# Kernel tuning notes

Measured on AMD Instinct MI355X. Metric: run time of the kernel, lower is better.

Reference implementation:

```python
import jax, jax.numpy as jnp
import numpy as np

NEG_SLOPE = 0.2   # negative_slope
EPS = 1e-6        # leaky-relu eps
BN_EPS = 1e-5     # torch BatchNorm default eps


def setup_inputs() -> dict:
    key = jax.random.key(0)
    k1, k2, k3 = jax.random.split(key, 3)
    B, C_in, C_out, N = 8, 256, 256, 8192
    x = jax.random.normal(k1, (B, C_in, 3, N), dtype=jnp.float32)
    s = 1.0 / np.sqrt(C_in)  # nn.Linear default init range
    W_feat = jax.random.uniform(k2, (C_out, C_in), minval=-s, maxval=s, dtype=jnp.float32)
    W_dir = jax.random.uniform(k3, (C_out, C_in), minval=-s, maxval=s, dtype=jnp.float32)
    gamma = jnp.ones((C_out,), jnp.float32)
    beta = jnp.zeros((C_out,), jnp.float32)
    return {"x": x, "W_feat": W_feat, "W_dir": W_dir, "gamma": gamma, "beta": beta}


def reference(x, W_feat, W_dir, gamma, beta):
    # VNLinear: kron(W, eye(3)) conv2d == per-vector channel mix
    p = jnp.einsum('oc,bcdn->bodn', W_feat, x)  # [B, O, 3, N]

    # VNBatchNorm: BN (training mode, batch stats) on vector norms, then rescale
    norm = jnp.sqrt(jnp.sum(p * p, axis=2))           # [B, O, N]
    mean = jnp.mean(norm, axis=(0, 2))                # [O]
    var = jnp.var(norm, axis=(0, 2))                  # [O] biased, as torch BN
    norm_bn = ((norm - mean[None, :, None]) * jax.lax.rsqrt(var + BN_EPS)[None, :, None]
               * gamma[None, :, None] + beta[None, :, None])
    p = p / norm[:, :, None, :] * norm_bn[:, :, None, :]

    # VNLeakyReLU with direction computed from the ORIGINAL input x
    d = jnp.einsum('oc,bcdn->bodn', W_dir, x)         # [B, O, 3, N]
    dot = jnp.sum(p * d, axis=2, keepdims=True)       # [B, O, 1, N]
    d_norm_sq = jnp.sum(d * d, axis=2, keepdims=True)
    return jnp.where(dot >= 0, p, p - (1.0 - NEG_SLOPE) * (dot / (d_norm_sq + EPS)) * d)
```

## Files before the change

### kernel.cpp

```cpp
#include <hip/hip_runtime.h>
#include <math.h>

#define BDIM 8
#define CIN  256
#define COUT 256
#define NDIM 8192

#define NEG_COEF  0.8f
#define LRELU_EPS 1e-6f
#define BN_EPS    1e-5f

typedef __attribute__((ext_vector_type(8))) short bf16x8;
typedef __attribute__((ext_vector_type(4))) float f32x4;

#define WS_WFH 0
#define WS_WFL 65536
#define WS_WDH 131072
#define WS_WDL 196608
#define WS_STATS_BYTE 524288
#define NSLOT 8
#define TILE_BYTES 12288
#define WS_XHI_BYTE 557056
#define XIMG_BYTES 100663296ull
#define WS_XLO_BYTE (WS_XHI_BYTE + XIMG_BYTES)
#define WS_NEED (WS_XLO_BYTE + XIMG_BYTES)

__device__ __forceinline__ unsigned short f2bf(float f) {
    unsigned u = __float_as_uint(f);
    return (unsigned short)((u + 0x7FFFu + ((u >> 16) & 1u)) >> 16);
}
__device__ __forceinline__ float bf2f(unsigned short h) {
    return __uint_as_float(((unsigned)h) << 16);
}

__device__ __forceinline__ int swz(int off) {
    return off ^ (((off >> 6) & 7) << 4);
}

__device__ __forceinline__ void gl_lds16(const char* g, char* l) {
    __builtin_amdgcn_global_load_lds(
        (const __attribute__((address_space(1))) unsigned int*)g,
        (__attribute__((address_space(3))) unsigned int*)l, 16, 0, 0);
}

__global__ __launch_bounds__(256) void setup_w_kernel(
    const float* __restrict__ Wf, const float* __restrict__ Wd,
    unsigned short* __restrict__ wsu)
{
    const int o = blockIdx.x;
    const int mat = blockIdx.y;
    const int c = threadIdx.x;
    const float* W = mat ? Wd : Wf;
    float w = W[o * CIN + c];
    unsigned short hi = f2bf(w);
    unsigned short lo = f2bf(w - bf2f(hi));
    int pos = (c & ~31) + 4 * (c & 7) + ((c >> 3) & 3);
    unsigned short* ph = wsu + (mat ? WS_WDH : WS_WFH);
    unsigned short* pl = wsu + (mat ? WS_WDL : WS_WFL);
    ph[o * CIN + pos] = hi;
    pl[o * CIN + pos] = lo;
}

__global__ __launch_bounds__(256) void vn_convert(
    const float* __restrict__ x,
    char* __restrict__ xh, char* __restrict__ xl)
{
    const int t    = threadIdx.x;
    const int nblk = blockIdx.x;
    const int ct   = blockIdx.y;
    const int b    = blockIdx.z;
    const int n0   = nblk * 64;
    const int c0   = ct * 32;

    char* gh = xh + ((size_t)(b * 128 + nblk)) * (8 * TILE_BYTES) + ct * TILE_BYTES;
    char* gl = xl + ((size_t)(b * 128 + nblk)) * (8 * TILE_BYTES) + ct * TILE_BYTES;

    #pragma unroll
    for (int p = 0; p < 3; ++p) {
        const int m  = p * 256 + t;
        const int dr = m >> 2, dp = m & 3;
        const int sr = (dr & ~1) | ((dr ^ (dr >> 2)) & 1);
        const int sp = dp ^ (sr & 3);
        const int d  = sr >> 6, nl = sr & 63;
        const int kb = sp * 2;
        float v[8];
        #pragma unroll
        for (int i = 0; i < 4; ++i) {
            const float* base = x + ((size_t)((b * CIN + c0 + kb + 8 * i) * 3 + d)) * NDIM + n0 + nl;
            v[i]     = base[0];
            v[4 + i] = base[3 * NDIM];
        }
        unsigned short h[8];
        #pragma unroll
        for (int j = 0; j < 8; ++j) h[j] = f2bf(v[j]);
        uint4 H = make_uint4((unsigned)h[0] | ((unsigned)h[1] << 16),
                             (unsigned)h[2] | ((unsigned)h[3] << 16),
                             (unsigned)h[4] | ((unsigned)h[5] << 16),
                             (unsigned)h[6] | ((unsigned)h[7] << 16));
        unsigned short lo[8];
        #pragma unroll
        for (int j = 0; j < 8; ++j) lo[j] = f2bf(v[j] - bf2f(h[j]));
        uint4 L = make_uint4((unsigned)lo[0] | ((unsigned)lo[1] << 16),
                             (unsigned)lo[2] | ((unsigned)lo[3] << 16),
                             (unsigned)lo[4] | ((unsigned)lo[5] << 16),
                             (unsigned)lo[6] | ((unsigned)lo[7] << 16));
        *(uint4*)(gh + m * 16) = H;
        *(uint4*)(gl + m * 16) = L;
    }
}

__device__ __forceinline__ void stats_step(
    int ct, const char* gh, const char* srd, char* swr,
    int t, int q, int ln, int oo,
    const unsigned short* wfh, f32x4 (*acc)[12])
{
    if (ct < 7) {
        #pragma unroll
        for (int p = 0; p < 3; ++p)
            gl_lds16(gh + (ct + 1) * TILE_BYTES + t * 16 + p * 4096,
                     swr + t * 16 + p * 4096);
    }
    bf16x8 af[2];
    #pragma unroll
    for (int mt = 0; mt < 2; ++mt)
        af[mt] = *(const bf16x8*)&wfh[(oo + mt * 16 + ln) * CIN + ct * 32 + q * 8];
    #pragma unroll
    for (int nt = 0; nt < 12; ++nt) {
        bf16x8 bh = *(const bf16x8*)(srd + swz((nt * 16 + ln) * 64 + q * 16));
        #pragma unroll
        for (int mt = 0; mt < 2; ++mt)
            acc[mt][nt] = __builtin_amdgcn_mfma_f32_16x16x32_bf16(af[mt], bh, acc[mt][nt], 0, 0, 0);
    }
    __syncthreads();
}

__global__ __launch_bounds__(256) void vn_stats2(
    const unsigned short* __restrict__ wsu, const char* __restrict__ xh,
    float* __restrict__ stats)
{
    __shared__ uint4 sA4[TILE_BYTES / 16];
    __shared__ uint4 sB4[TILE_BYTES / 16];
    __shared__ float redS[128], redQ[128];
    char* sA = (char*)sA4;
    char* sB = (char*)sB4;

    const int t    = threadIdx.x;
    const int nblk = blockIdx.x;
    const int oy   = blockIdx.y;
    const int b    = blockIdx.z;

    const int lane = t & 63;
    const int w    = t >> 6;
    const int q    = lane >> 4;
    const int ln   = lane & 15;
    const int oo   = oy * 128 + w * 32;

    if (t < 128) { redS[t] = 0.f; redQ[t] = 0.f; }

    f32x4 acc[2][12];
    #pragma unroll
    for (int i = 0; i < 2; ++i)
        #pragma unroll
        for (int j = 0; j < 12; ++j) acc[i][j] = (f32x4)0.f;

    const unsigned short* wfh = wsu + WS_WFH;
    const char* gh = xh + ((size_t)(b * 128 + nblk)) * (8 * TILE_BYTES);

    #pragma unroll
    for (int p = 0; p < 3; ++p)
        gl_lds16(gh + t * 16 + p * 4096, sA + t * 16 + p * 4096);
    __syncthreads();

    for (int cp = 0; cp < 4; ++cp) {
        stats_step(2 * cp,     gh, sA, sB, t, q, ln, oo, wfh, acc);
        stats_step(2 * cp + 1, gh, sB, sA, t, q, ln, oo, wfh, acc);
    }

    #pragma unroll
    for (int mt = 0; mt < 2; ++mt) {
        #pragma unroll
        for (int r = 0; r < 4; ++r) {
            float s = 0.f, s2 = 0.f;
            #pragma unroll
            for (int h = 0; h < 4; ++h) {
                float p0 = acc[mt][0 + h][r];
                float p1 = acc[mt][4 + h][r];
                float p2 = acc[mt][8 + h][r];
                float n2 = p0 * p0 + p1 * p1 + p2 * p2;
                s += sqrtf(n2); s2 += n2;
            }
            #pragma unroll
            for (int m = 1; m < 16; m <<= 1) {
                s  += __shfl_xor(s,  m, 64);
                s2 += __shfl_xor(s2, m, 64);
            }
            if (ln == 0) {
                int ol = w * 32 + mt * 16 + q * 4 + r;
                atomicAdd(&redS[ol], s);
                atomicAdd(&redQ[ol], s2);
            }
        }
    }
    __syncthreads();
    if (t < 128) {
        int slot = nblk & (NSLOT - 1);
        atomicAdd(&stats[slot * 256 + oy * 128 + t], redS[t]);
        atomicAdd(&stats[NSLOT * 256 + slot * 256 + oy * 128 + t], redQ[t]);
    }
}

__global__ __launch_bounds__(256) void vn_finalize2(
    float* __restrict__ stats, const float* __restrict__ gamma)
{
    int o = threadIdx.x;
    float s = 0.f, s2 = 0.f;
    #pragma unroll
    for (int i = 0; i < NSLOT; ++i) {
        s  += stats[i * 256 + o];
        s2 += stats[(NSLOT + i) * 256 + o];
    }
    const float inv = 1.0f / (float)(BDIM * NDIM);
    float mean = s * inv;
    float var  = fmaxf(s2 * inv - mean * mean, 0.f);
    stats[2 * NSLOT * 256 + o] = mean;
    stats[2 * NSLOT * 256 + 256 + o] = gamma[o] * rsqrtf(var + BN_EPS);
}

__device__ __forceinline__ void main_step(
    int ct, const char* ghb, const char* glb,
    const char* shr, const char* slr, char* shw, char* slw,
    int t, int q, int ln, int oo, int nb,
    const unsigned short* wfh, const unsigned short* wfl,
    const unsigned short* wdh, const unsigned short* wdl,
    f32x4 (*accP)[6], f32x4 (*accD)[6])
{
    if (ct < 7) {
        #pragma unroll
        for (int p = 0; p < 3; ++p) {
            gl_lds16(ghb + (ct + 1) * TILE_BYTES + t * 16 + p * 4096,
                     shw + t * 16 + p * 4096);
            gl_lds16(glb + (ct + 1) * TILE_BYTES + t * 16 + p * 4096,
                     slw + t * 16 + p * 4096);
        }
    }
    const int c0 = ct * 32;
    bf16x8 afh[2], afl[2], adh[2], adl[2];
    #pragma unroll
    for (int mt = 0; mt < 2; ++mt) {
        const int row = (oo + mt * 16 + ln) * CIN + c0 + q * 8;
        afh[mt] = *(const bf16x8*)&wfh[row];
        afl[mt] = *(const bf16x8*)&wfl[row];
        adh[mt] = *(const bf16x8*)&wdh[row];
        adl[mt] = *(const bf16x8*)&wdl[row];
    }
    #pragma unroll
    for (int nt = 0; nt < 6; ++nt) {
        const int d = nt >> 1, h = nt & 1;
        const int jloc = d * 64 + nb + h * 16 + ln;
        const int off = swz(jloc * 64 + q * 16);
        bf16x8 bh = *(const bf16x8*)(shr + off);
        bf16x8 bl = *(const bf16x8*)(slr + off);
        #pragma unroll
        for (int mt = 0; mt < 2; ++mt) {
            f32x4 aP = accP[mt][nt];
            aP = __builtin_amdgcn_mfma_f32_16x16x32_bf16(afh[mt], bh, aP, 0, 0, 0);
            aP = __builtin_amdgcn_mfma_f32_16x16x32_bf16(afh[mt], bl, aP, 0, 0, 0);
            aP = __builtin_amdgcn_mfma_f32_16x16x32_bf16(afl[mt], bh, aP, 0, 0, 0);
            aP = __builtin_amdgcn_mfma_f32_16x16x32_bf16(afl[mt], bl, aP, 0, 0, 0);
            accP[mt][nt] = aP;
            f32x4 aD = accD[mt][nt];
            aD = __builtin_amdgcn_mfma_f32_16x16x32_bf16(adh[mt], bh, aD, 0, 0, 0);
            aD = __builtin_amdgcn_mfma_f32_16x16x32_bf16(adh[mt], bl, aD, 0, 0, 0);
            aD = __builtin_amdgcn_mfma_f32_16x16x32_bf16(adl[mt], bh, aD, 0, 0, 0);
            accD[mt][nt] = aD;
        }
    }
    __syncthreads();
}

__global__ __launch_bounds__(256) void vn_main3(
    const unsigned short* __restrict__ wsu,
    const char* __restrict__ xh, const char* __restrict__ xl,
    const float* __restrict__ stats, const float* __restrict__ beta,
    float* __restrict__ out)
{
    __shared__ uint4 sHA4[TILE_BYTES / 16];
    __shared__ uint4 sHB4[TILE_BYTES / 16];
    __shared__ uint4 sLA4[TILE_BYTES / 16];
    __shared__ uint4 sLB4[TILE_BYTES / 16];
    char* sHA = (char*)sHA4;
    char* sHB = (char*)sHB4;
    char* sLA = (char*)sLA4;
    char* sLB = (char*)sLB4;

    const int t    = threadIdx.x;
    const int nblk = blockIdx.x;
    const int n0   = nblk * 64;
    const int o0   = blockIdx.y * 64;
    const int b    = blockIdx.z;

    const int lane = t & 63;
    const int w    = t >> 6;
    const int q    = lane >> 4;
    const int ln   = lane & 15;

    f32x4 accP[2][6], accD[2][6];
    #pragma unroll
    for (int i = 0; i < 2; ++i)
        #pragma unroll
        for (int j = 0; j < 6; ++j) { accP[i][j] = (f32x4)0.f; accD[i][j] = (f32x4)0.f; }

    const unsigned short* wfh = wsu + WS_WFH;
    const unsigned short* wfl = wsu + WS_WFL;
    const unsigned short* wdh = wsu + WS_WDH;
    const unsigned short* wdl = wsu + WS_WDL;
    const int oo = o0 + (w >> 1) * 32;
    const int nb = (w & 1) * 32;

    const char* ghb = xh + ((size_t)(b * 128 + nblk)) * (8 * TILE_BYTES);
    const char* glb = xl + ((size_t)(b * 128 + nblk)) * (8 * TILE_BYTES);

    #pragma unroll
    for (int p = 0; p < 3; ++p) {
        gl_lds16(ghb + t * 16 + p * 4096, sHA + t * 16 + p * 4096);
        gl_lds16(glb + t * 16 + p * 4096, sLA + t * 16 + p * 4096);
    }
    __syncthreads();

    for (int cp = 0; cp < 4; ++cp) {
        main_step(2 * cp,     ghb, glb, sHA, sLA, sHB, sLB,
                  t, q, ln, oo, nb, wfh, wfl, wdh, wdl, accP, accD);
        main_step(2 * cp + 1, ghb, glb, sHB, sLB, sHA, sLA,
                  t, q, ln, oo, nb, wfh, wfl, wdh, wdl, accP, accD);
    }

    const float* meanp  = stats + 2 * NSLOT * 256;
    const float* scalep = meanp + 256;
    #pragma unroll
    for (int mt = 0; mt < 2; ++mt) {
        #pragma unroll
        for (int r = 0; r < 4; ++r) {
            const int o = oo + mt * 16 + q * 4 + r;
            const float mean  = meanp[o];
            const float scale = scalep[o];
            const float bet   = beta[o];
            #pragma unroll
            for (int h = 0; h < 2; ++h) {
                float p0 = accP[mt][0 + h][r], p1 = accP[mt][2 + h][r], p2 = accP[mt][4 + h][r];
                float d0 = accD[mt][0 + h][r], d1 = accD[mt][2 + h][r], d2 = accD[mt][4 + h][r];
                float n2 = p0 * p0 + p1 * p1 + p2 * p2;
                float nr = sqrtf(n2);
                float f  = ((nr - mean) * scale + bet) / nr;
                p0 *= f; p1 *= f; p2 *= f;
                float dot = p0 * d0 + p1 * d1 + p2 * d2;
                if (dot < 0.f) {
                    float g = NEG_COEF * dot / (d0 * d0 + d1 * d1 + d2 * d2 + LRELU_EPS);
                    p0 -= g * d0; p1 -= g * d1; p2 -= g * d2;
                }
                const int n = n0 + nb + h * 16 + ln;
                out[((size_t)(b * COUT + o) * 3 + 0) * NDIM + n] = p0;
                out[((size_t)(b * COUT + o) * 3 + 1) * NDIM + n] = p1;
                out[((size_t)(b * COUT + o) * 3 + 2) * NDIM + n] = p2;
            }
        }
    }
}

__global__ __launch_bounds__(256) void vn_stats_mfma(
    const float* __restrict__ x, const unsigned short* __restrict__ wsu,
    float* __restrict__ stats)
{
    __shared__ unsigned short sXhi[192 * 40];
    __shared__ float redS[64], redQ[64];

    const int t  = threadIdx.x;
    const int n0 = blockIdx.x * 64;
    const int o0 = blockIdx.y * 64;
    const int b  = blockIdx.z;

    const int lane = t & 63;
    const int w    = t >> 6;
    const int q    = lane >> 4;
    const int ln   = lane & 15;

    const int jl = t & 31;
    const int kb = t >> 5;

    if (t < 64) { redS[t] = 0.f; redQ[t] = 0.f; }

    f32x4 acc[2][6];
    #pragma unroll
    for (int i = 0; i < 2; ++i)
        #pragma unroll
        for (int j = 0; j < 6; ++j) acc[i][j] = (f32x4)0.f;

    const unsigned short* wfh = wsu + WS_WFH;
    const int oo = o0 + (w >> 1) * 32;
    const int nb = (w & 1) * 32;

    for (int c0 = 0; c0 < CIN; c0 += 32) {
        __syncthreads();
        #pragma unroll
        for (int ip = 0; ip < 6; ++ip) {
            int jloc = ip * 32 + jl;
            int d = jloc >> 6, nl = jloc & 63;
            float v[4];
            #pragma unroll
            for (int i = 0; i < 4; ++i) {
                int c = c0 + kb + 8 * i;
                v[i] = x[((size_t)((b * CIN + c) * 3 + d)) * NDIM + n0 + nl];
            }
            unsigned p0 = (unsigned)f2bf(v[0]) | ((unsigned)f2bf(v[1]) << 16);
            unsigned p1 = (unsigned)f2bf(v[2]) | ((unsigned)f2bf(v[3]) << 16);
            *(uint2*)&sXhi[jloc * 40 + kb * 4] = make_uint2(p0, p1);
        }
        __syncthreads();
        bf16x8 af[2];
        #pragma unroll
        for (int mt = 0; mt < 2; ++mt)
            af[mt] = *(const bf16x8*)&wfh[(oo + mt * 16 + ln) * CIN + c0 + q * 8];
        #pragma unroll
        for (int nt = 0; nt < 6; ++nt) {
            int d = nt >> 1, h = nt & 1;
            int jloc = d * 64 + nb + h * 16 + ln;
            bf16x8 bh = *(const bf16x8*)&sXhi[jloc * 40 + q * 8];
            #pragma unroll
            for (int mt = 0; mt < 2; ++mt)
                acc[mt][nt] = __builtin_amdgcn_mfma_f32_16x16x32_bf16(af[mt], bh, acc[mt][nt], 0, 0, 0);
        }
    }

    #pragma unroll
    for (int mt = 0; mt < 2; ++mt) {
        #pragma unroll
        for (int r = 0; r < 4; ++r) {
            float s = 0.f, s2 = 0.f;
            #pragma unroll
            for (int h = 0; h < 2; ++h) {
                float p0 = acc[mt][0 + h][r];
                float p1 = acc[mt][2 + h][r];
                float p2 = acc[mt][4 + h][r];
                float n2 = p0 * p0 + p1 * p1 + p2 * p2;
                s += sqrtf(n2); s2 += n2;
            }
            #pragma unroll
            for (int m = 1; m < 16; m <<= 1) {
                s  += __shfl_xor(s,  m, 64);
                s2 += __shfl_xor(s2, m, 64);
            }
            if (ln == 0) {
                int ol = (w >> 1) * 32 + mt * 16 + q * 4 + r;
                atomicAdd(&redS[ol], s);
                atomicAdd(&redQ[ol], s2);
            }
        }
    }
    __syncthreads();
    if (t < 64) {
        int slot = blockIdx.x & (NSLOT - 1);
        atomicAdd(&stats[slot * 256 + o0 + t], redS[t]);
        atomicAdd(&stats[NSLOT * 256 + slot * 256 + o0 + t], redQ[t]);
    }
}

__global__ __launch_bounds__(256) void vn_main_mfma(
    const float* __restrict__ x, const unsigned short* __restrict__ wsu,
    const float* __restrict__ stats, const float* __restrict__ beta,
    float* __restrict__ out)
{
    __shared__ unsigned short sXhi[192 * 40];
    __shared__ unsigned short sXlo[192 * 40];

    const int t  = threadIdx.x;
    const int n0 = blockIdx.x * 64;
    const int o0 = blockIdx.y * 64;
    const int b  = blockIdx.z;

    const int lane = t & 63;
    const int w    = t >> 6;
    const int q    = lane >> 4;
    const int ln   = lane & 15;

    const int jl = t & 31;
    const int kb = t >> 5;

    f32x4 accP[2][6], accD[2][6];
    #pragma unroll
    for (int i = 0; i < 2; ++i)
        #pragma unroll
        for (int j = 0; j < 6; ++j) { accP[i][j] = (f32x4)0.f; accD[i][j] = (f32x4)0.f; }

    const unsigned short* wfh = wsu + WS_WFH;
    const unsigned short* wfl = wsu + WS_WFL;
    const unsigned short* wdh = wsu + WS_WDH;
    const unsigned short* wdl = wsu + WS_WDL;
    const int oo = o0 + (w >> 1) * 32;
    const int nb = (w & 1) * 32;

    for (int c0 = 0; c0 < CIN; c0 += 32) {
        __syncthreads();
        #pragma unroll
        for (int ip = 0; ip < 6; ++ip) {
            int jloc = ip * 32 + jl;
            int d = jloc >> 6, nl = jloc & 63;
            float v[4];
            #pragma unroll
            for (int i = 0; i < 4; ++i) {
                int c = c0 + kb + 8 * i;
                v[i] = x[((size_t)((b * CIN + c) * 3 + d)) * NDIM + n0 + nl];
            }
            unsigned short h0 = f2bf(v[0]), h1 = f2bf(v[1]), h2 = f2bf(v[2]), h3 = f2bf(v[3]);
            unsigned ph0 = (unsigned)h0 | ((unsigned)h1 << 16);
            unsigned ph1 = (unsigned)h2 | ((unsigned)h3 << 16);
            unsigned pl0 = (unsigned)f2bf(v[0] - bf2f(h0)) | ((unsigned)f2bf(v[1] - bf2f(h1)) << 16);
            unsigned pl1 = (unsigned)f2bf(v[2] - bf2f(h2)) | ((unsigned)f2bf(v[3] - bf2f(h3)) << 16);
            *(uint2*)&sXhi[jloc * 40 + kb * 4] = make_uint2(ph0, ph1);
            *(uint2*)&sXlo[jloc * 40 + kb * 4] = make_uint2(pl0, pl1);
        }
        __syncthreads();
        bf16x8 afh[2], afl[2], adh[2], adl[2];
        #pragma unroll
        for (int mt = 0; mt < 2; ++mt) {
            int row = (oo + mt * 16 + ln) * CIN + c0 + q * 8;
            afh[mt] = *(const bf16x8*)&wfh[row];
            afl[mt] = *(const bf16x8*)&wfl[row];
            adh[mt] = *(const bf16x8*)&wdh[row];
            adl[mt] = *(const bf16x8*)&wdl[row];
        }
        #pragma unroll
        for (int nt = 0; nt < 6; ++nt) {
            int d = nt >> 1, h = nt & 1;
            int jloc = d * 64 + nb + h * 16 + ln;
            bf16x8 bh = *(const bf16x8*)&sXhi[jloc * 40 + q * 8];
            bf16x8 bl = *(const bf16x8*)&sXlo[jloc * 40 + q * 8];
            #pragma unroll
            for (int mt = 0; mt < 2; ++mt) {
                f32x4 aP = accP[mt][nt];
                aP = __builtin_amdgcn_mfma_f32_16x16x32_bf16(afh[mt], bh, aP, 0, 0, 0);
                aP = __builtin_amdgcn_mfma_f32_16x16x32_bf16(afh[mt], bl, aP, 0, 0, 0);
                aP = __builtin_amdgcn_mfma_f32_16x16x32_bf16(afl[mt], bh, aP, 0, 0, 0);
                aP = __builtin_amdgcn_mfma_f32_16x16x32_bf16(afl[mt], bl, aP, 0, 0, 0);
                accP[mt][nt] = aP;
                f32x4 aD = accD[mt][nt];
                aD = __builtin_amdgcn_mfma_f32_16x16x32_bf16(adh[mt], bh, aD, 0, 0, 0);
                aD = __builtin_amdgcn_mfma_f32_16x16x32_bf16(adh[mt], bl, aD, 0, 0, 0);
                aD = __builtin_amdgcn_mfma_f32_16x16x32_bf16(adl[mt], bh, aD, 0, 0, 0);
                accD[mt][nt] = aD;
            }
        }
    }

    const float* meanp  = stats + 2 * NSLOT * 256;
    const float* scalep = meanp + 256;
    #pragma unroll
    for (int mt = 0; mt < 2; ++mt) {
        #pragma unroll
        for (int r = 0; r < 4; ++r) {
            const int o = oo + mt * 16 + q * 4 + r;
            const float mean  = meanp[o];
            const float scale = scalep[o];
            const float bet   = beta[o];
            #pragma unroll
            for (int h = 0; h < 2; ++h) {
                float p0 = accP[mt][0 + h][r], p1 = accP[mt][2 + h][r], p2 = accP[mt][4 + h][r];
                float d0 = accD[mt][0 + h][r], d1 = accD[mt][2 + h][r], d2 = accD[mt][4 + h][r];
                float n2 = p0 * p0 + p1 * p1 + p2 * p2;
                float nr = sqrtf(n2);
                float f  = ((nr - mean) * scale + bet) / nr;
                p0 *= f; p1 *= f; p2 *= f;
                float dot = p0 * d0 + p1 * d1 + p2 * d2;
                if (dot < 0.f) {
                    float g = NEG_COEF * dot / (d0 * d0 + d1 * d1 + d2 * d2 + LRELU_EPS);
                    p0 -= g * d0; p1 -= g * d1; p2 -= g * d2;
                }
                const int n = n0 + nb + h * 16 + ln;
                out[((size_t)(b * COUT + o) * 3 + 0) * NDIM + n] = p0;
                out[((size_t)(b * COUT + o) * 3 + 1) * NDIM + n] = p1;
                out[((size_t)(b * COUT + o) * 3 + 2) * NDIM + n] = p2;
            }
        }
    }
}

extern "C" void kernel_launch(void* const* d_in, const int* in_sizes, int n_in,
                              void* d_out, int out_size, void* d_ws, size_t ws_size,
                              hipStream_t stream) {
    const float* x     = (const float*)d_in[0];
    const float* Wf    = (const float*)d_in[1];
    const float* Wd    = (const float*)d_in[2];
    const float* gamma = (const float*)d_in[3];
    const float* beta  = (const float*)d_in[4];
    float* out = (float*)d_out;
    unsigned short* wsu = (unsigned short*)d_ws;
    float* stats = (float*)((char*)d_ws + WS_STATS_BYTE);

    hipMemsetAsync((char*)d_ws + WS_STATS_BYTE, 0, 2 * NSLOT * 256 * sizeof(float), stream);
    setup_w_kernel<<<dim3(256, 2), 256, 0, stream>>>(Wf, Wd, wsu);

    if (ws_size >= (size_t)WS_NEED) {
        char* xhp = (char*)d_ws + WS_XHI_BYTE;
        char* xlp = (char*)d_ws + WS_XLO_BYTE;
        vn_convert<<<dim3(128, 8, 8), 256, 0, stream>>>(x, xhp, xlp);
        vn_stats2<<<dim3(128, 2, 8), 256, 0, stream>>>(wsu, xhp, stats);
        vn_finalize2<<<1, 256, 0, stream>>>(stats, gamma);
        vn_main3<<<dim3(128, 4, 8), 256, 0, stream>>>(wsu, xhp, xlp, stats, beta, out);
    } else {
        dim3 grid(NDIM / 64, COUT / 64, BDIM);
        vn_stats_mfma<<<grid, 256, 0, stream>>>(x, wsu, stats);
        vn_finalize2<<<1, 256, 0, stream>>>(stats, gamma);
        vn_main_mfma<<<grid, 256, 0, stream>>>(x, wsu, stats, beta, out);
    }
}
```

Measured before the change: 632.2 us.

## Fuse bf16 split conversion with BN statistics GEMM into one kernel

Merges the x-to-bf16 hi/lo conversion kernel and the batch-norm statistics GEMM into a single 512-thread kernel. Each block stages fp32 x tiles through shared memory with coalesced float4 loads, builds the swizzled bf16 tile in LDS for its own MFMAs, and writes the hi/lo images to global for the main kernel. This removes the stats kernel re-reading the hi image from global and one launch, and each block now covers all 256 output channels, so x is read once. The cost is that prefetch overlap is limited to register double-buffering, and there are fewer, larger blocks, which lowers parallelism.

After: 612.8 us. 1.03x faster.

```diff
diff --git a/kernel.cpp b/kernel.cpp
--- a/kernel.cpp
+++ b/kernel.cpp
@@ -24,6 +24,8 @@
 #define XIMG_BYTES 100663296ull
 #define WS_XLO_BYTE (WS_XHI_BYTE + XIMG_BYTES)
 #define WS_NEED (WS_XLO_BYTE + XIMG_BYTES)
+
+#define XT_PITCH 68
 
 __device__ __forceinline__ unsigned short f2bf(float f) {
     unsigned u = __float_as_uint(f);
@@ -61,101 +63,62 @@
     pl[o * CIN + pos] = lo;
 }
 
-__global__ __launch_bounds__(256) void vn_convert(
-    const float* __restrict__ x,
-    char* __restrict__ xh, char* __restrict__ xl)
-{
+__device__ __forceinline__ void build_chunk(
+    int m, const float* __restrict__ xs, char* __restrict__ img,
+    char* __restrict__ gh, char* __restrict__ gl)
+{
+    const int dr = m >> 2, dp = m & 3;
+    const int sr = (dr & ~1) | ((dr ^ (dr >> 2)) & 1);
+    const int sp = dp ^ (sr & 3);
+    const int d  = sr >> 6, nl = sr & 63;
+    const int kb = sp * 2;
+    float v[8];
+    #pragma unroll
+    for (int i = 0; i < 4; ++i) {
+        v[i]     = xs[((kb + 8 * i) * 3 + d) * XT_PITCH + nl];
+        v[4 + i] = xs[((kb + 1 + 8 * i) * 3 + d) * XT_PITCH + nl];
+    }
+    unsigned short h[8];
+    #pragma unroll
+    for (int j = 0; j < 8; ++j) h[j] = f2bf(v[j]);
+    uint4 H = make_uint4((unsigned)h[0] | ((unsigned)h[1] << 16),
+                         (unsigned)h[2] | ((unsigned)h[3] << 16),
+                         (unsigned)h[4] | ((unsigned)h[5] << 16),
+                         (unsigned)h[6] | ((unsigned)h[7] << 16));
+    unsigned short lo[8];
+    #pragma unroll
+    for (int j = 0; j < 8; ++j) lo[j] = f2bf(v[j] - bf2f(h[j]));
+    uint4 L = make_uint4((unsigned)lo[0] | ((unsigned)lo[1] << 16),
+                         (unsigned)lo[2] | ((unsigned)lo[3] << 16),
+                         (unsigned)lo[4] | ((unsigned)lo[5] << 16),
+                         (unsigned)lo[6] | ((unsigned)lo[7] << 16));
+    *(uint4*)(img + m * 16) = H;
+    *(uint4*)(gh + m * 16)  = H;
+    *(uint4*)(gl + m * 16)  = L;
+}
+
+__global__ __launch_bounds__(512) void vn_cvtstats(
+    const float* __restrict__ x, const unsigned short* __restrict__ wsu,
+    char* __restrict__ xh, char* __restrict__ xl,
+    float* __restrict__ stats)
+{
+    __shared__ float xs[96 * XT_PITCH];
+    __shared__ uint4 img4[TILE_BYTES / 16];
+    __shared__ float redS[256], redQ[256];
+    char* img = (char*)img4;
+
     const int t    = threadIdx.x;
     const int nblk = blockIdx.x;
-    const int ct   = blockIdx.y;
     const int b    = blockIdx.z;
     const int n0   = nblk * 64;
-    const int c0   = ct * 32;
-
-    char* gh = xh + ((size_t)(b * 128 + nblk)) * (8 * TILE_BYTES) + ct * TILE_BYTES;
-    char* gl = xl + ((size_t)(b * 128 + nblk)) * (8 * TILE_BYTES) + ct * TILE_BYTES;
-
-    #pragma unroll
-    for (int p = 0; p < 3; ++p) {
-        const int m  = p * 256 + t;
-        const int dr = m >> 2, dp = m & 3;
-        const int sr = (dr & ~1) | ((dr ^ (dr >> 2)) & 1);
-        const int sp = dp ^ (sr & 3);
-        const int d  = sr >> 6, nl = sr & 63;
-        const int kb = sp * 2;
-        float v[8];
-        #pragma unroll
-        for (int i = 0; i < 4; ++i) {
-            const float* base = x + ((size_t)((b * CIN + c0 + kb + 8 * i) * 3 + d)) * NDIM + n0 + nl;
-            v[i]     = base[0];
-            v[4 + i] = base[3 * NDIM];
-        }
-        unsigned short h[8];
-        #pragma unroll
-        for (int j = 0; j < 8; ++j) h[j] = f2bf(v[j]);
-        uint4 H = make_uint4((unsigned)h[0] | ((unsigned)h[1] << 16),
-                             (unsigned)h[2] | ((unsigned)h[3] << 16),
-                             (unsigned)h[4] | ((unsigned)h[5] << 16),
-                             (unsigned)h[6] | ((unsigned)h[7] << 16));
-        unsigned short lo[8];
-        #pragma unroll
-        for (int j = 0; j < 8; ++j) lo[j] = f2bf(v[j] - bf2f(h[j]));
-        uint4 L = make_uint4((unsigned)lo[0] | ((unsigned)lo[1] << 16),
-                             (unsigned)lo[2] | ((unsigned)lo[3] << 16),
-                             (unsigned)lo[4] | ((unsigned)lo[5] << 16),
-                             (unsigned)lo[6] | ((unsigned)lo[7] << 16));
-        *(uint4*)(gh + m * 16) = H;
-        *(uint4*)(gl + m * 16) = L;
-    }
-}
-
-__device__ __forceinline__ void stats_step(
-    int ct, const char* gh, const char* srd, char* swr,
-    int t, int q, int ln, int oo,
-    const unsigned short* wfh, f32x4 (*acc)[12])
-{
-    if (ct < 7) {
-        #pragma unroll
-        for (int p = 0; p < 3; ++p)
-            gl_lds16(gh + (ct + 1) * TILE_BYTES + t * 16 + p * 4096,
-                     swr + t * 16 + p * 4096);
-    }
-    bf16x8 af[2];
-    #pragma unroll
-    for (int mt = 0; mt < 2; ++mt)
-        af[mt] = *(const bf16x8*)&wfh[(oo + mt * 16 + ln) * CIN + ct * 32 + q * 8];
-    #pragma unroll
-    for (int nt = 0; nt < 12; ++nt) {
-        bf16x8 bh = *(const bf16x8*)(srd + swz((nt * 16 + ln) * 64 + q * 16));
-        #pragma unroll
-        for (int mt = 0; mt < 2; ++mt)
-            acc[mt][nt] = __builtin_amdgcn_mfma_f32_16x16x32_bf16(af[mt], bh, acc[mt][nt], 0, 0, 0);
-    }
-    __syncthreads();
-}
-
-__global__ __launch_bounds__(256) void vn_stats2(
-    const unsigned short* __restrict__ wsu, const char* __restrict__ xh,
-    float* __restrict__ stats)
-{
-    __shared__ uint4 sA4[TILE_BYTES / 16];
-    __shared__ uint4 sB4[TILE_BYTES / 16];
-    __shared__ float redS[128], redQ[128];
-    char* sA = (char*)sA4;
-    char* sB = (char*)sB4;
-
-    const int t    = threadIdx.x;
-    const int nblk = blockIdx.x;
-    const int oy   = blockIdx.y;
-    const int b    = blockIdx.z;
 
     const int lane = t & 63;
     const int w    = t >> 6;
     const int q    = lane >> 4;
     const int ln   = lane & 15;
-    const int oo   = oy * 128 + w * 32;
-
-    if (t < 128) { redS[t] = 0.f; redQ[t] = 0.f; }
+    const int oo   = w * 32;
+
+    if (t < 256) { redS[t] = 0.f; redQ[t] = 0.f; }
 
     f32x4 acc[2][12];
     #pragma unroll
@@ -164,16 +127,51 @@
         for (int j = 0; j < 12; ++j) acc[i][j] = (f32x4)0.f;
 
     const unsigned short* wfh = wsu + WS_WFH;
-    const char* gh = xh + ((size_t)(b * 128 + nblk)) * (8 * TILE_BYTES);
-
-    #pragma unroll
-    for (int p = 0; p < 3; ++p)
-        gl_lds16(gh + t * 16 + p * 4096, sA + t * 16 + p * 4096);
-    __syncthreads();
-
-    for (int cp = 0; cp < 4; ++cp) {
-        stats_step(2 * cp,     gh, sA, sB, t, q, ln, oo, wfh, acc);
-        stats_step(2 * cp + 1, gh, sB, sA, t, q, ln, oo, wfh, acc);
+    char* ghb = xh + ((size_t)(b * 128 + nblk)) * (8 * TILE_BYTES);
+    char* glb = xl + ((size_t)(b * 128 + nblk)) * (8 * TILE_BYTES);
+    const float* xb0 = x + ((size_t)(b * CIN) * 3) * NDIM + n0;
+
+    float4 xr[3];
+    #pragma unroll
+    for (int k = 0; k < 3; ++k) {
+        const int idx = k * 512 + t;
+        const int row = idx >> 4, col = idx & 15;
+        xr[k] = *(const float4*)(xb0 + (size_t)row * NDIM + col * 4);
+    }
+
+    for (int ct = 0; ct < 8; ++ct) {
+        __syncthreads();
+        #pragma unroll
+        for (int k = 0; k < 3; ++k) {
+            const int idx = k * 512 + t;
+            const int row = idx >> 4, col = idx & 15;
+            *(float4*)&xs[row * XT_PITCH + col * 4] = xr[k];
+        }
+        __syncthreads();
+        build_chunk(t, xs, img, ghb + ct * TILE_BYTES, glb + ct * TILE_BYTES);
+        if (t < 256)
+            build_chunk(512 + t, xs, img, ghb + ct * TILE_BYTES, glb + ct * TILE_BYTES);
+        __syncthreads();
+        if (ct < 7) {
+            const float* xbn = xb0 + (size_t)(ct + 1) * 32 * 3 * NDIM;
+            #pragma unroll
+            for (int k = 0; k < 3; ++k) {
+                const int idx = k * 512 + t;
+                const int row = idx >> 4, col = idx & 15;
+                xr[k] = *(const float4*)(xbn + (size_t)row * NDIM + col * 4);
+            }
+        }
+        bf16x8 af[2];
+        #pragma unroll
+        for (int mt = 0; mt < 2; ++mt)
+            af[mt] = *(const bf16x8*)&wfh[(oo + mt * 16 + ln) * CIN + ct * 32 + q * 8];
+        #pragma unroll
+        for (int nt = 0; nt < 12; ++nt) {
+            bf16x8 bh = *(const bf16x8*)(img + swz((nt * 16 + ln) * 64 + q * 16));
+            #pragma unroll
+            for (int mt = 0; mt < 2; ++mt)
+                acc[mt][nt] = __builtin_amdgcn_mfma_f32_16x16x32_bf16(af[mt], bh, acc[mt][nt], 0, 0, 0);
+        }
     }
 
     #pragma unroll
@@ -195,17 +193,17 @@
                 s2 += __shfl_xor(s2, m, 64);
             }
             if (ln == 0) {
-                int ol = w * 32 + mt * 16 + q * 4 + r;
-                atomicAdd(&redS[ol], s);
-                atomicAdd(&redQ[ol], s2);
+                int o = oo + mt * 16 + q * 4 + r;
+                atomicAdd(&redS[o], s);
+                atomicAdd(&redQ[o], s2);
             }
         }
     }
     __syncthreads();
-    if (t < 128) {
+    if (t < 256) {
         int slot = nblk & (NSLOT - 1);
-        atomicAdd(&stats[slot * 256 + oy * 128 + t], redS[t]);
-        atomicAdd(&stats[NSLOT * 256 + slot * 256 + oy * 128 + t], redQ[t]);
+        atomicAdd(&stats[slot * 256 + t], redS[t]);
+        atomicAdd(&stats[NSLOT * 256 + slot * 256 + t], redQ[t]);
     }
 }
 
@@ -600,8 +598,7 @@
     if (ws_size >= (size_t)WS_NEED) {
         char* xhp = (char*)d_ws + WS_XHI_BYTE;
         char* xlp = (char*)d_ws + WS_XLO_BYTE;
-        vn_convert<<<dim3(128, 8, 8), 256, 0, stream>>>(x, xhp, xlp);
-        vn_stats2<<<dim3(128, 2, 8), 256, 0, stream>>>(wsu, xhp, stats);
+        vn_cvtstats<<<dim3(128, 1, 8), 512, 0, stream>>>(x, wsu, xhp, xlp, stats);
         vn_finalize2<<<1, 256, 0, stream>>>(stats, gamma);
         vn_main3<<<dim3(128, 4, 8), 256, 0, stream>>>(wsu, xhp, xlp, stats, beta, out);
     } else {
```
